# Kernel optimization log

Measured on AMD Instinct MI355X. Metric: run time of the kernel, lower is better.

The kernel has to match this reference:

```python
import jax, jax.numpy as jnp
import numpy as np

SIGMAS = (1.0, 10.0, 100.0, 1000.0)
EPS_RATIO = 1e-3  # lambda ridge term and ratio clip epsilon


def euclidsq(x, y):
    # squared pairwise Euclidean distances, [m, n]
    d = jnp.sum(x * x, axis=-1)[:, None] + jnp.sum(y * y, axis=-1)[None, :] - 2.0 * (x @ y.T)
    return jnp.maximum(d, 0.0)


def kmm_ratio(Kdede, Kdenu, lam):
    # original: inv(Kdede + lam*I) @ Kdenu @ ones == solve(A, Kdenu @ ones)
    n_de = Kdede.shape[0]
    A = Kdede + lam * jnp.eye(n_de, dtype=Kdede.dtype)
    B = jnp.sum(Kdenu, axis=1, keepdims=True)  # [n_de, 1]
    return jnp.linalg.solve(A, B)


def estimate_ratio(x_de, x_nu):
    # averaged KMM ratio over Gaussian kernels with fixed sigmas, then clip
    dsq_dede = euclidsq(x_de, x_de)
    dsq_denu = euclidsq(x_de, x_nu)
    ratio = 0.0
    for s in SIGMAS:
        inv2s2 = 1.0 / (2.0 * s * s)
        Kdede = jnp.exp(-dsq_dede * inv2s2)
        Kdenu = jnp.exp(-dsq_denu * inv2s2)
        ratio = ratio + kmm_ratio(Kdede, Kdenu, EPS_RATIO)
    ratio = ratio / len(SIGMAS)
    return jax.nn.relu(ratio) + EPS_RATIO  # clip_ratio=True


def reference(z1, z2, perm1, perm2):
    n, d = z1.shape
    z1s, z2s = z1[perm1], z2[perm2]
    # numerator ratio over full concatenated embeddings
    num_ratio = estimate_ratio(jnp.concatenate([z1, z2], axis=-1),
                               jnp.concatenate([z1s, z2s], axis=-1))
    num_ratio = 1.0 / num_ratio  # [n, 1]
    x_nu = jnp.concatenate([z2, z2], axis=-1)  # constant across samples

    def per_sample(z1_i):
        # x_de row j = concat(z1_i, z2_shuffled[j])
        x_de = jnp.concatenate([jnp.broadcast_to(z1_i, (n, d)), z2s], axis=-1)
        return jnp.sum(estimate_ratio(x_de, x_nu))

    denum_sums = jax.vmap(per_sample)(z1)  # [n]
    loss = jnp.sum(-jnp.log(num_ratio[:, 0] / denum_sums))
    return loss


def setup_inputs() -> dict:
    key = jax.random.key(0)
    k1, k2 = jax.random.split(key)
    n, d = 256, 128
    z1 = jax.random.normal(k1, (n, d), dtype=jnp.float32)
    z2 = jax.random.normal(k2, (n, d), dtype=jnp.float32)
    perm1 = jnp.arange(n, dtype=jnp.int32)
    perm2 = jnp.arange(n, dtype=jnp.int32)
    return {"z1": z1, "z2": z2, "perm1": perm1, "perm2": perm2}
```

## Files before the change

kernel.cpp:

```cpp
#include <hip/hip_runtime.h>
#include <math.h>

#define N 256
#define Dd 128

__device__ __forceinline__ double inv2s2_of(int s){
    return (s==0)?0.5:(s==1)?5.0e-3:(s==2)?5.0e-5:5.0e-7;
}

__device__ __forceinline__ void sweep32(double P[32][33], int tid){
    if (tid < 64){
        int r = tid & 31, cg = tid >> 5;
        for (int j = 0; j < 32; j++){
            double d    = P[j][j];
            double invd = 1.0 / d;
            double cr   = P[r][j];
            double s    = cr * invd;
            bool rj = (r == j);
            double nv[16];
            #pragma unroll
            for (int c = 0; c < 16; c++){
                int col = cg*16 + c;
                double pj = P[j][col];
                double v  = P[r][col];
                nv[c] = rj ? ((col == j) ? -invd : v * invd)
                           : ((col == j) ? s : v - s*pj);
            }
            #pragma unroll
            for (int c = 0; c < 16; c++) P[r][cg*16+c] = nv[c];
        }
        #pragma unroll
        for (int c = 0; c < 16; c++) P[r][cg*16+c] = -P[r][cg*16+c];
    }
}

__global__ void k_dist(const float* __restrict__ z1, const float* __restrict__ z2,
                       const int* __restrict__ p1, const int* __restrict__ p2,
                       double* __restrict__ Aden, double* __restrict__ Anum,
                       double* __restrict__ S0, float* __restrict__ M4,
                       float* __restrict__ U4, double* __restrict__ bnum){
    __shared__ float Xs[16][17], Ys[16][17];
    int w = blockIdx.z;
    int tx = threadIdx.x, ty = threadIdx.y;
    int row = blockIdx.y*16 + ty, col = blockIdx.x*16 + tx;
    const float *Xb[2], *Yb[2]; const int *Xp[2], *Yp[2]; int npair = 1;
    Xb[1]=0; Yb[1]=0; Xp[0]=0; Yp[0]=0; Xp[1]=0; Yp[1]=0;
    switch(w){
        case 0: Xb[0]=z1; Yb[0]=z1; Xb[1]=z2; Yb[1]=z2; npair=2; break;
        case 1: Xb[0]=z1; Yb[0]=z1; Yp[0]=p1; Xb[1]=z2; Yb[1]=z2; Yp[1]=p2; npair=2; break;
        case 2: Xb[0]=z2; Yb[0]=z2; Xp[0]=p2; Yp[0]=p2; break;
        case 3: Xb[0]=z2; Yb[0]=z2; Xp[0]=p2; break;
        default:Xb[0]=z1; Yb[0]=z2; break;
    }
    double acc = 0.0;
    for (int p = 0; p < npair; p++){
        const float* X = Xb[p]; const float* Y = Yb[p];
        int xr = blockIdx.y*16 + ty; if (Xp[p]) xr = Xp[p][xr];
        int yr = blockIdx.x*16 + ty; if (Yp[p]) yr = Yp[p][yr];
        for (int c = 0; c < Dd; c += 16){
            __syncthreads();
            Xs[ty][tx] = X[xr*Dd + c + tx];
            Ys[ty][tx] = Y[yr*Dd + c + tx];
            __syncthreads();
            #pragma unroll
            for (int t = 0; t < 16; t++){
                float d = Xs[ty][t] - Ys[tx][t];
                acc += (double)d * (double)d;
            }
        }
    }
    int o = row*N + col;
    if (w == 0){
        #pragma unroll
        for (int s = 0; s < 4; s++){
            double v = exp(-inv2s2_of(s)*acc);
            if (row == col) v += 1.0e-3;
            Anum[s*N*N + o] = v;
            S0[(4+s)*N*N + o] = v;
        }
    } else if (w == 1){
        #pragma unroll
        for (int s = 0; s < 4; s++){
            double v = exp(-inv2s2_of(s)*acc);
            v += __shfl_down(v, 8, 16);
            v += __shfl_down(v, 4, 16);
            v += __shfl_down(v, 2, 16);
            v += __shfl_down(v, 1, 16);
            if (tx == 0) atomicAdd(&bnum[s*N + row], v);
        }
    } else if (w == 2){
        #pragma unroll
        for (int s = 0; s < 4; s++){
            double v = exp(-inv2s2_of(s)*acc);
            if (row == col) v += 1.0e-3;
            Aden[s*N*N + o] = v;
            S0[s*N*N + o] = v;
        }
    } else if (w == 3){
        #pragma unroll
        for (int s = 0; s < 4; s++) M4[s*N*N + o] = (float)exp(-inv2s2_of(s)*acc);
    } else {
        #pragma unroll
        for (int s = 0; s < 4; s++) U4[s*N*N + o] = (float)exp(-inv2s2_of(s)*acc);
    }
}


__global__ void k_pivot0(const double* __restrict__ S0, double* __restrict__ Pg0){
    __shared__ double P[32][33];
    int mat = blockIdx.x;
    const double* S = S0 + (size_t)mat*65536;
    double* Pp = Pg0 + (size_t)mat*1024;
    int tid = threadIdx.x;
    #pragma unroll
    for (int l = 0; l < 4; l++){
        int e = tid + l*256; P[e>>5][e&31] = S[(size_t)(e>>5)*N + (e&31)];
    }
    __syncthreads();
    sweep32(P, tid);
    __syncthreads();
    #pragma unroll
    for (int l = 0; l < 4; l++){
        int e = tid + l*256; Pp[e] = P[e>>5][e&31];
    }
}

__global__ void k_step(const double* __restrict__ Ssrc, double* __restrict__ Sdst,
                       const double* __restrict__ PgS, double* __restrict__ PgD, int k){
    __shared__ double Pl[32][33], EJ[32][33], Cl[32][33], El[32][33];
    int bx = blockIdx.x, mat = blockIdx.y;
    const double* S = Ssrc + (size_t)mat*65536;
    double* D = Sdst + (size_t)mat*65536;
    const double* Pp = PgS + (size_t)mat*1024;
    int tid = threadIdx.x;
    int Kb = k*32;
    #pragma unroll
    for (int l = 0; l < 4; l++){
        int e = tid + l*256; Pl[e>>5][e&31] = Pp[e];
    }
    if (bx < 49){
        int I = bx / 7, J = bx % 7;
        int GI = ((I < k) ? I : I + 1) * 32;
        int GJ = ((J < k) ? J : J + 1) * 32;
        #pragma unroll
        for (int l = 0; l < 4; l++){
            int e = tid + l*256; int r = e >> 5, c = e & 31;
            El[r][c] = S[(size_t)(GI + r)*N + Kb + c];
            EJ[r][c] = S[(size_t)(GJ + r)*N + Kb + c];
        }
        __syncthreads();
        #pragma unroll
        for (int l = 0; l < 4; l++){
            int e = tid + l*256; int r = e >> 5, c = e & 31;
            double acc = 0.0;
            #pragma unroll
            for (int kk = 0; kk < 32; kk++) acc += EJ[r][kk] * Pl[kk][c];
            Cl[r][c] = acc;
        }
        __syncthreads();
        int pr = tid >> 4, pc = tid & 15;
        int r0 = 2*pr, c0 = 2*pc;
        double a00 = S[(size_t)(GI+r0)*N + GJ+c0];
        double a01 = S[(size_t)(GI+r0)*N + GJ+c0+1];
        double a10 = S[(size_t)(GI+r0+1)*N + GJ+c0];
        double a11 = S[(size_t)(GI+r0+1)*N + GJ+c0+1];
        #pragma unroll
        for (int kk = 0; kk < 32; kk++){
            double e0 = El[r0][kk],   e1 = El[r0+1][kk];
            double b0 = Cl[c0][kk],   b1 = Cl[c0+1][kk];
            a00 -= e0*b0; a01 -= e0*b1;
            a10 -= e1*b0; a11 -= e1*b1;
        }
        double* Dp = D + (size_t)(GI + r0)*N + GJ + c0;
        Dp[0]   = a00; Dp[1]   = a01;
        Dp[N]   = a10; Dp[N+1] = a11;
        if (I == k && J == k && k < 7){
            __syncthreads();
            El[r0][c0]   = a00; El[r0][c0+1]   = a01;
            El[r0+1][c0] = a10; El[r0+1][c0+1] = a11;
            __syncthreads();
            sweep32(El, tid);
            __syncthreads();
            double* Pd = PgD + (size_t)mat*1024;
            #pragma unroll
            for (int l = 0; l < 4; l++){
                int e = tid + l*256; Pd[e] = El[e>>5][e&31];
            }
        }
    } else {
        int T = bx - 49;
        int GT = ((T < k) ? T : T + 1) * 32;
        #pragma unroll
        for (int l = 0; l < 4; l++){
            int e = tid + l*256; int r = e >> 5, c = e & 31;
            El[r][c] = S[(size_t)(GT + r)*N + Kb + c];
        }
        __syncthreads();
        #pragma unroll
        for (int l = 0; l < 4; l++){
            int e = tid + l*256; int r = e >> 5, c = e & 31;
            double acc = 0.0;
            #pragma unroll
            for (int kk = 0; kk < 32; kk++) acc += El[r][kk] * Pl[kk][c];
            Cl[r][c] = acc;
        }
        __syncthreads();
        #pragma unroll
        for (int l = 0; l < 4; l++){
            int e = tid + l*256; int r = e >> 5, c = e & 31;
            D[(size_t)(GT + r)*N + Kb + c] = Cl[r][c];
        }
        #pragma unroll
        for (int l = 0; l < 4; l++){
            int e = tid + l*256; int cc = e >> 5, rr = e & 31;
            D[(size_t)(Kb + cc)*N + GT + rr] = Cl[rr][cc];
        }
        if (T == 0){
            #pragma unroll
            for (int l = 0; l < 4; l++){
                int e = tid + l*256; int i = e >> 5, j = e & 31;
                D[(size_t)(Kb + i)*N + Kb + j] = -Pl[i][j];
            }
        }
    }
}

__global__ void k_gemm_nt(const float* __restrict__ M4, const float* __restrict__ U4,
                          double* __restrict__ Bmat){
    int s = blockIdx.z;
    const float* Mp = M4 + s*N*N;
    const float* Up = U4 + s*N*N;
    double* Bp = Bmat + s*N*N;
    __shared__ float Ms[32][33], Us[32][33];
    int tx = threadIdx.x, ty = threadIdx.y;
    int tid = ty*16 + tx;
    int bj = blockIdx.y*32, bi = blockIdx.x*32;
    double a00=0, a01=0, a10=0, a11=0;
    for (int kc = 0; kc < N; kc += 32){
        __syncthreads();
        #pragma unroll
        for (int l = 0; l < 4; l++){
            int e = tid + l*256; int r = e >> 5, c = e & 31;
            Ms[r][c] = Mp[(bj+r)*N + kc + c];
            Us[r][c] = Up[(bi+r)*N + kc + c];
        }
        __syncthreads();
        #pragma unroll
        for (int k = 0; k < 32; k++){
            float x0 = Ms[2*ty][k], x1 = Ms[2*ty+1][k];
            float y0 = Us[2*tx][k], y1 = Us[2*tx+1][k];
            a00 += (double)x0*y0; a01 += (double)x0*y1;
            a10 += (double)x1*y0; a11 += (double)x1*y1;
        }
    }
    Bp[(bj+2*ty  )*N + bi+2*tx  ] = a00;
    Bp[(bj+2*ty  )*N + bi+2*tx+1] = a01;
    Bp[(bj+2*ty+1)*N + bi+2*tx  ] = a10;
    Bp[(bj+2*ty+1)*N + bi+2*tx+1] = a11;
}

__global__ void k_gemm_x0(const double* __restrict__ Sfin, const double* __restrict__ Bmat,
                          float* __restrict__ X0){
    int s = blockIdx.z;
    const double* Sp = Sfin + (size_t)s*N*N;
    const double* Bp = Bmat + s*N*N;
    float* Xp = X0 + s*N*N;
    __shared__ float Gs[32][33];
    __shared__ double Bs[32][33];
    int tx = threadIdx.x, ty = threadIdx.y;
    int tid = ty*16 + tx;
    int bj = blockIdx.y*32, bi = blockIdx.x*32;
    double a00=0, a01=0, a10=0, a11=0;
    for (int kc = 0; kc < N; kc += 32){
        __syncthreads();
        #pragma unroll
        for (int l = 0; l < 4; l++){
            int e = tid + l*256; int r = e >> 5, c = e & 31;
            Gs[r][c] = -(float)Sp[(size_t)(bj+r)*N + kc + c];
            Bs[r][c] = Bp[(kc+r)*N + bi + c];
        }
        __syncthreads();
        #pragma unroll
        for (int k = 0; k < 32; k++){
            float x0 = Gs[2*ty][k], x1 = Gs[2*ty+1][k];
            double y0 = Bs[k][2*tx], y1 = Bs[k][2*tx+1];
            a00 += (double)x0*y0; a01 += (double)x0*y1;
            a10 += (double)x1*y0; a11 += (double)x1*y1;
        }
    }
    Xp[(bj+2*ty  )*N + bi+2*tx  ] = (float)a00;
    Xp[(bj+2*ty  )*N + bi+2*tx+1] = (float)a01;
    Xp[(bj+2*ty+1)*N + bi+2*tx  ] = (float)a10;
    Xp[(bj+2*ty+1)*N + bi+2*tx+1] = (float)a11;
}

__global__ void k_gemm_r(const double* __restrict__ Aden, const float* __restrict__ X0,
                         const double* __restrict__ Bmat, float* __restrict__ Rm){
    int s = blockIdx.z;
    const double* Ap = Aden + s*N*N;
    const float* Xp = X0 + s*N*N;
    const double* Bp = Bmat + s*N*N;
    float* Rp = Rm + s*N*N;
    __shared__ double As[32][33];
    __shared__ float Xs[32][33];
    int tx = threadIdx.x, ty = threadIdx.y;
    int tid = ty*16 + tx;
    int bj = blockIdx.y*32, bi = blockIdx.x*32;
    double a00=0, a01=0, a10=0, a11=0;
    for (int kc = 0; kc < N; kc += 32){
        __syncthreads();
        #pragma unroll
        for (int l = 0; l < 4; l++){
            int e = tid + l*256; int r = e >> 5, c = e & 31;
            As[r][c] = Ap[(bj+r)*N + kc + c];
            Xs[r][c] = Xp[(kc+r)*N + bi + c];
        }
        __syncthreads();
        #pragma unroll
        for (int k = 0; k < 32; k++){
            double x0 = As[2*ty][k], x1 = As[2*ty+1][k];
            double y0 = (double)Xs[k][2*tx], y1 = (double)Xs[k][2*tx+1];
            a00 += x0*y0; a01 += x0*y1;
            a10 += x1*y0; a11 += x1*y1;
        }
    }
    int r0 = bj+2*ty, c0 = bi+2*tx;
    Rp[(r0  )*N + c0  ] = (float)(Bp[(r0  )*N + c0  ] - a00);
    Rp[(r0  )*N + c0+1] = (float)(Bp[(r0  )*N + c0+1] - a01);
    Rp[(r0+1)*N + c0  ] = (float)(Bp[(r0+1)*N + c0  ] - a10);
    Rp[(r0+1)*N + c0+1] = (float)(Bp[(r0+1)*N + c0+1] - a11);
}

__global__ void k_gemm_xl(const double* __restrict__ Sfin, const float* __restrict__ Rm,
                          const float* __restrict__ X0, double* __restrict__ dsum,
                          const double* __restrict__ Anum,
                          const double* __restrict__ bnum, float* __restrict__ rnum){
    __shared__ float Gs[32][33], Rs[32][33];
    __shared__ double cp[16][33];
    __shared__ double y0[256], rr2[256], bsh[256];
    int tx = threadIdx.x, ty = threadIdx.y;
    int tid = ty*16 + tx;
    if (blockIdx.y == 8){
        if (blockIdx.x >= 4) return;
        int s = blockIdx.x, j = tid;
        const double* Sn = Sfin + (size_t)(4+s)*N*N;
        const double* Ap = Anum + s*N*N;
        const double* bp = bnum + s*N;
        bsh[j] = bp[j];
        __syncthreads();
        double acc = 0;
        for (int k = 0; k < N; k++) acc -= Sn[(size_t)k*N+j] * bsh[k];
        y0[j] = acc;
        __syncthreads();
        acc = 0;
        for (int k = 0; k < N; k++) acc += Ap[(size_t)k*N+j] * y0[k];
        rr2[j] = bsh[j] - acc;
        __syncthreads();
        acc = 0;
        for (int k = 0; k < N; k++) acc -= Sn[(size_t)k*N+j] * rr2[k];
        rnum[s*N+j] = (float)(y0[j] + acc);
        return;
    }
    int bj = blockIdx.y*32, bi = blockIdx.x*32;
    int r0 = bj+2*ty, c0 = bi+2*tx;
    double s00=0, s01=0, s10=0, s11=0;
    for (int s = 0; s < 4; s++){
        const double* Sp = Sfin + (size_t)s*N*N;
        const float* Rp = Rm + s*N*N;
        const float* X0p = X0 + s*N*N;
        double a00=0, a01=0, a10=0, a11=0;
        for (int kc = 0; kc < N; kc += 32){
            __syncthreads();
            #pragma unroll
            for (int l = 0; l < 4; l++){
                int e = tid + l*256; int r = e >> 5, c = e & 31;
                Gs[r][c] = -(float)Sp[(size_t)(bj+r)*N + kc + c];
                Rs[r][c] = Rp[(kc+r)*N + bi + c];
            }
            __syncthreads();
            #pragma unroll
            for (int k = 0; k < 32; k++){
                float x0 = Gs[2*ty][k], x1 = Gs[2*ty+1][k];
                float y0v = Rs[k][2*tx], y1v = Rs[k][2*tx+1];
                a00 += (double)x0*y0v; a01 += (double)x0*y1v;
                a10 += (double)x1*y0v; a11 += (double)x1*y1v;
            }
        }
        s00 += (double)X0p[(r0  )*N + c0  ] + a00;
        s01 += (double)X0p[(r0  )*N + c0+1] + a01;
        s10 += (double)X0p[(r0+1)*N + c0  ] + a10;
        s11 += (double)X0p[(r0+1)*N + c0+1] + a11;
    }
    double v00 = (double)fmaxf((float)(0.25*s00), 0.f);
    double v01 = (double)fmaxf((float)(0.25*s01), 0.f);
    double v10 = (double)fmaxf((float)(0.25*s10), 0.f);
    double v11 = (double)fmaxf((float)(0.25*s11), 0.f);
    __syncthreads();
    cp[ty][2*tx]   = v00 + v10;
    cp[ty][2*tx+1] = v01 + v11;
    __syncthreads();
    if (tid < 32){
        double ssum = 0;
        #pragma unroll
        for (int t = 0; t < 16; t++) ssum += cp[t][tid];
        atomicAdd(&dsum[bi + tid], ssum);
    }
}

__global__ void k_loss2(const double* __restrict__ dsum, const float* __restrict__ rnum,
                        float* __restrict__ out){
    __shared__ double red[256];
    int i = threadIdx.x;
    double denum = dsum[i] + (double)N * 1.0e-3;
    float ravg = 0.25f*(rnum[0*N+i] + rnum[1*N+i] + rnum[2*N+i] + rnum[3*N+i]);
    double rn = (double)fmaxf(ravg, 0.f) + 1.0e-3;
    red[i] = log(rn) + log(denum);
    __syncthreads();
    for (int st = 128; st > 0; st >>= 1){
        if (i < st) red[i] += red[i + st];
        __syncthreads();
    }
    if (i == 0) out[0] = (float)red[0];
}

extern "C" void kernel_launch(void* const* d_in, const int* in_sizes, int n_in,
                              void* d_out, int out_size, void* d_ws, size_t ws_size,
                              hipStream_t stream) {
    (void)in_sizes; (void)n_in; (void)out_size; (void)ws_size;
    const float* z1 = (const float*)d_in[0];
    const float* z2 = (const float*)d_in[1];
    const int*   p1 = (const int*)d_in[2];
    const int*   p2 = (const int*)d_in[3];
    float* out = (float*)d_out;

    char* w = (char*)d_ws;
    size_t o = 0;
    auto carve = [&](size_t bytes) -> char* {
        char* p = w + o;
        o += (bytes + 255) & ~(size_t)255;
        return p;
    };
    double*   bnum = (double*) carve((size_t)4*N*sizeof(double));
    double*   dsum = (double*) carve((size_t)N*sizeof(double));
    size_t zbytes = o;
    double* Aden = (double*)carve((size_t)4*N*N*sizeof(double));
    double* Anum = (double*)carve((size_t)4*N*N*sizeof(double));
    float*  M4   = (float*) carve((size_t)4*N*N*sizeof(float));
    float*  U4   = (float*) carve((size_t)4*N*N*sizeof(float));
    double* Bmat = (double*)carve((size_t)4*N*N*sizeof(double));
    float*  X0   = (float*) carve((size_t)4*N*N*sizeof(float));
    float*  Rm   = (float*) carve((size_t)4*N*N*sizeof(float));
    float*  rnum = (float*) carve((size_t)4*N*sizeof(float));
    double* S0   = (double*)carve((size_t)8*N*N*sizeof(double));
    double* S1   = (double*)carve((size_t)8*N*N*sizeof(double));
    double* Pg0  = (double*)carve((size_t)8*32*32*sizeof(double));
    double* Pg1  = (double*)carve((size_t)8*32*32*sizeof(double));

    hipMemsetAsync(d_ws, 0, zbytes, stream);
    k_dist<<<dim3(16,16,5), dim3(16,16), 0, stream>>>(z1, z2, p1, p2,
                                                      Aden, Anum, S0, M4, U4, bnum);
    k_gemm_nt<<<dim3(8,8,4), dim3(16,16), 0, stream>>>(M4, U4, Bmat);
    k_pivot0<<<dim3(8), dim3(256), 0, stream>>>(S0, Pg0);
    for (int k = 0; k < 8; k++){
        double* src = (k & 1) ? S1 : S0;
        double* dst = (k & 1) ? S0 : S1;
        double* ps  = (k & 1) ? Pg1 : Pg0;
        double* pd  = (k & 1) ? Pg0 : Pg1;
        k_step<<<dim3(56,8), dim3(256), 0, stream>>>(src, dst, ps, pd, k);
    }
    k_gemm_x0<<<dim3(8,8,4), dim3(16,16), 0, stream>>>(S0, Bmat, X0);
    k_gemm_r<<<dim3(8,8,4), dim3(16,16), 0, stream>>>(Aden, X0, Bmat, Rm);
    k_gemm_xl<<<dim3(8,9), dim3(16,16), 0, stream>>>(S0, Rm, X0, dsum,
                                                     Anum, bnum, rnum);
    k_loss2<<<dim3(1), dim3(256), 0, stream>>>(dsum, rnum, out);
}
```

Baseline: 495.1 us.

## Drop iterative refinement pass, fuse pivot into gemm, and remove memset via partial sums

Removes the residual-refinement stage (the k_gemm_r and k_gemm_xl correction GEMMs and the Anum/Aden copies) and computes the solution with a single double-precision inverse-times-B GEMM followed by a reduction kernel. The first pivot sweep is folded into the k_gemm_nt launch as an extra z-slice, which also zeroes dsum. bnum atomics are replaced by per-block partial sums, so the memset goes away. Three launches and several large intermediate buffers are eliminated. The cost is dropping the refinement step, which may reduce solution accuracy for the ill-conditioned large-sigma kernels.

```diff
diff --git a/kernel.cpp b/kernel.cpp
--- a/kernel.cpp
+++ b/kernel.cpp
@@ -36,9 +36,8 @@
 
 __global__ void k_dist(const float* __restrict__ z1, const float* __restrict__ z2,
                        const int* __restrict__ p1, const int* __restrict__ p2,
-                       double* __restrict__ Aden, double* __restrict__ Anum,
                        double* __restrict__ S0, float* __restrict__ M4,
-                       float* __restrict__ U4, double* __restrict__ bnum){
+                       float* __restrict__ U4, double* __restrict__ bpart){
     __shared__ float Xs[16][17], Ys[16][17];
     int w = blockIdx.z;
     int tx = threadIdx.x, ty = threadIdx.y;
@@ -75,8 +74,7 @@
         for (int s = 0; s < 4; s++){
             double v = exp(-inv2s2_of(s)*acc);
             if (row == col) v += 1.0e-3;
-            Anum[s*N*N + o] = v;
-            S0[(4+s)*N*N + o] = v;
+            S0[(size_t)(4+s)*N*N + o] = v;
         }
     } else if (w == 1){
         #pragma unroll
@@ -86,15 +84,14 @@
             v += __shfl_down(v, 4, 16);
             v += __shfl_down(v, 2, 16);
             v += __shfl_down(v, 1, 16);
-            if (tx == 0) atomicAdd(&bnum[s*N + row], v);
+            if (tx == 0) bpart[((size_t)s*N + row)*16 + blockIdx.x] = v;
         }
     } else if (w == 2){
         #pragma unroll
         for (int s = 0; s < 4; s++){
             double v = exp(-inv2s2_of(s)*acc);
             if (row == col) v += 1.0e-3;
-            Aden[s*N*N + o] = v;
-            S0[s*N*N + o] = v;
+            S0[(size_t)s*N*N + o] = v;
         }
     } else if (w == 3){
         #pragma unroll
@@ -105,24 +102,59 @@
     }
 }
 
-
-__global__ void k_pivot0(const double* __restrict__ S0, double* __restrict__ Pg0){
+__global__ void k_gemm_nt(const float* __restrict__ M4, const float* __restrict__ U4,
+                          double* __restrict__ Bmat, const double* __restrict__ S0,
+                          double* __restrict__ Pg0, double* __restrict__ dsum){
+    __shared__ float Ms[32][33], Us[32][33];
     __shared__ double P[32][33];
-    int mat = blockIdx.x;
-    const double* S = S0 + (size_t)mat*65536;
-    double* Pp = Pg0 + (size_t)mat*1024;
-    int tid = threadIdx.x;
-    #pragma unroll
-    for (int l = 0; l < 4; l++){
-        int e = tid + l*256; P[e>>5][e&31] = S[(size_t)(e>>5)*N + (e&31)];
-    }
-    __syncthreads();
-    sweep32(P, tid);
-    __syncthreads();
-    #pragma unroll
-    for (int l = 0; l < 4; l++){
-        int e = tid + l*256; Pp[e] = P[e>>5][e&31];
-    }
+    int tx = threadIdx.x, ty = threadIdx.y;
+    int tid = ty*16 + tx;
+    if (blockIdx.z == 4){
+        if (blockIdx.y != 0) return;
+        int mat = blockIdx.x;
+        if (mat == 0) dsum[tid] = 0.0;
+        const double* S = S0 + (size_t)mat*65536;
+        #pragma unroll
+        for (int l = 0; l < 4; l++){
+            int e = tid + l*256; P[e>>5][e&31] = S[(size_t)(e>>5)*N + (e&31)];
+        }
+        __syncthreads();
+        sweep32(P, tid);
+        __syncthreads();
+        double* Pp = Pg0 + (size_t)mat*1024;
+        #pragma unroll
+        for (int l = 0; l < 4; l++){
+            int e = tid + l*256; Pp[e] = P[e>>5][e&31];
+        }
+        return;
+    }
+    int s = blockIdx.z;
+    const float* Mp = M4 + s*N*N;
+    const float* Up = U4 + s*N*N;
+    double* Bp = Bmat + s*N*N;
+    int bj = blockIdx.y*32, bi = blockIdx.x*32;
+    double a00=0, a01=0, a10=0, a11=0;
+    for (int kc = 0; kc < N; kc += 32){
+        __syncthreads();
+        #pragma unroll
+        for (int l = 0; l < 4; l++){
+            int e = tid + l*256; int r = e >> 5, c = e & 31;
+            Ms[r][c] = Mp[(bj+r)*N + kc + c];
+            Us[r][c] = Up[(bi+r)*N + kc + c];
+        }
+        __syncthreads();
+        #pragma unroll
+        for (int k = 0; k < 32; k++){
+            float x0 = Ms[2*ty][k], x1 = Ms[2*ty+1][k];
+            float y0 = Us[2*tx][k], y1 = Us[2*tx+1][k];
+            a00 += (double)x0*y0; a01 += (double)x0*y1;
+            a10 += (double)x1*y0; a11 += (double)x1*y1;
+        }
+    }
+    Bp[(bj+2*ty  )*N + bi+2*tx  ] = a00;
+    Bp[(bj+2*ty  )*N + bi+2*tx+1] = a01;
+    Bp[(bj+2*ty+1)*N + bi+2*tx  ] = a10;
+    Bp[(bj+2*ty+1)*N + bi+2*tx+1] = a11;
 }
 
 __global__ void k_step(const double* __restrict__ Ssrc, double* __restrict__ Sdst,
@@ -225,13 +257,13 @@
     }
 }
 
-__global__ void k_gemm_nt(const float* __restrict__ M4, const float* __restrict__ U4,
-                          double* __restrict__ Bmat){
+__global__ void k_x(const double* __restrict__ Sfin, const double* __restrict__ Bmat,
+                    float* __restrict__ Xm){
     int s = blockIdx.z;
-    const float* Mp = M4 + s*N*N;
-    const float* Up = U4 + s*N*N;
-    double* Bp = Bmat + s*N*N;
-    __shared__ float Ms[32][33], Us[32][33];
+    const double* Sp = Sfin + (size_t)s*N*N;
+    const double* Bp = Bmat + (size_t)s*N*N;
+    float* Xp = Xm + (size_t)s*N*N;
+    __shared__ double Gs[32][33], Bs[32][33];
     int tx = threadIdx.x, ty = threadIdx.y;
     int tid = ty*16 + tx;
     int bj = blockIdx.y*32, bi = blockIdx.x*32;
@@ -241,51 +273,16 @@
         #pragma unroll
         for (int l = 0; l < 4; l++){
             int e = tid + l*256; int r = e >> 5, c = e & 31;
-            Ms[r][c] = Mp[(bj+r)*N + kc + c];
-            Us[r][c] = Up[(bi+r)*N + kc + c];
+            Gs[r][c] = -Sp[(size_t)(bj+r)*N + kc + c];
+            Bs[r][c] = Bp[(size_t)(kc+r)*N + bi + c];
         }
         __syncthreads();
         #pragma unroll
         for (int k = 0; k < 32; k++){
-            float x0 = Ms[2*ty][k], x1 = Ms[2*ty+1][k];
-            float y0 = Us[2*tx][k], y1 = Us[2*tx+1][k];
-            a00 += (double)x0*y0; a01 += (double)x0*y1;
-            a10 += (double)x1*y0; a11 += (double)x1*y1;
-        }
-    }
-    Bp[(bj+2*ty  )*N + bi+2*tx  ] = a00;
-    Bp[(bj+2*ty  )*N + bi+2*tx+1] = a01;
-    Bp[(bj+2*ty+1)*N + bi+2*tx  ] = a10;
-    Bp[(bj+2*ty+1)*N + bi+2*tx+1] = a11;
-}
-
-__global__ void k_gemm_x0(const double* __restrict__ Sfin, const double* __restrict__ Bmat,
-                          float* __restrict__ X0){
-    int s = blockIdx.z;
-    const double* Sp = Sfin + (size_t)s*N*N;
-    const double* Bp = Bmat + s*N*N;
-    float* Xp = X0 + s*N*N;
-    __shared__ float Gs[32][33];
-    __shared__ double Bs[32][33];
-    int tx = threadIdx.x, ty = threadIdx.y;
-    int tid = ty*16 + tx;
-    int bj = blockIdx.y*32, bi = blockIdx.x*32;
-    double a00=0, a01=0, a10=0, a11=0;
-    for (int kc = 0; kc < N; kc += 32){
-        __syncthreads();
-        #pragma unroll
-        for (int l = 0; l < 4; l++){
-            int e = tid + l*256; int r = e >> 5, c = e & 31;
-            Gs[r][c] = -(float)Sp[(size_t)(bj+r)*N + kc + c];
-            Bs[r][c] = Bp[(kc+r)*N + bi + c];
-        }
-        __syncthreads();
-        #pragma unroll
-        for (int k = 0; k < 32; k++){
-            float x0 = Gs[2*ty][k], x1 = Gs[2*ty+1][k];
+            double x0 = Gs[2*ty][k], x1 = Gs[2*ty+1][k];
             double y0 = Bs[k][2*tx], y1 = Bs[k][2*tx+1];
-            a00 += (double)x0*y0; a01 += (double)x0*y1;
-            a10 += (double)x1*y0; a11 += (double)x1*y1;
+            a00 += x0*y0; a01 += x0*y1;
+            a10 += x1*y0; a11 += x1*y1;
         }
     }
     Xp[(bj+2*ty  )*N + bi+2*tx  ] = (float)a00;
@@ -294,116 +291,40 @@
     Xp[(bj+2*ty+1)*N + bi+2*tx+1] = (float)a11;
 }
 
-__global__ void k_gemm_r(const double* __restrict__ Aden, const float* __restrict__ X0,
-                         const double* __restrict__ Bmat, float* __restrict__ Rm){
-    int s = blockIdx.z;
-    const double* Ap = Aden + s*N*N;
-    const float* Xp = X0 + s*N*N;
-    const double* Bp = Bmat + s*N*N;
-    float* Rp = Rm + s*N*N;
-    __shared__ double As[32][33];
-    __shared__ float Xs[32][33];
-    int tx = threadIdx.x, ty = threadIdx.y;
-    int tid = ty*16 + tx;
-    int bj = blockIdx.y*32, bi = blockIdx.x*32;
-    double a00=0, a01=0, a10=0, a11=0;
-    for (int kc = 0; kc < N; kc += 32){
-        __syncthreads();
-        #pragma unroll
-        for (int l = 0; l < 4; l++){
-            int e = tid + l*256; int r = e >> 5, c = e & 31;
-            As[r][c] = Ap[(bj+r)*N + kc + c];
-            Xs[r][c] = Xp[(kc+r)*N + bi + c];
-        }
-        __syncthreads();
-        #pragma unroll
-        for (int k = 0; k < 32; k++){
-            double x0 = As[2*ty][k], x1 = As[2*ty+1][k];
-            double y0 = (double)Xs[k][2*tx], y1 = (double)Xs[k][2*tx+1];
-            a00 += x0*y0; a01 += x0*y1;
-            a10 += x1*y0; a11 += x1*y1;
-        }
-    }
-    int r0 = bj+2*ty, c0 = bi+2*tx;
-    Rp[(r0  )*N + c0  ] = (float)(Bp[(r0  )*N + c0  ] - a00);
-    Rp[(r0  )*N + c0+1] = (float)(Bp[(r0  )*N + c0+1] - a01);
-    Rp[(r0+1)*N + c0  ] = (float)(Bp[(r0+1)*N + c0  ] - a10);
-    Rp[(r0+1)*N + c0+1] = (float)(Bp[(r0+1)*N + c0+1] - a11);
-}
-
-__global__ void k_gemm_xl(const double* __restrict__ Sfin, const float* __restrict__ Rm,
-                          const float* __restrict__ X0, double* __restrict__ dsum,
-                          const double* __restrict__ Anum,
-                          const double* __restrict__ bnum, float* __restrict__ rnum){
-    __shared__ float Gs[32][33], Rs[32][33];
-    __shared__ double cp[16][33];
-    __shared__ double y0[256], rr2[256], bsh[256];
-    int tx = threadIdx.x, ty = threadIdx.y;
-    int tid = ty*16 + tx;
-    if (blockIdx.y == 8){
-        if (blockIdx.x >= 4) return;
-        int s = blockIdx.x, j = tid;
+__global__ void k_red(const float* __restrict__ Xm, const double* __restrict__ Sfin,
+                      const double* __restrict__ bpart, double* __restrict__ dsum,
+                      float* __restrict__ rnum){
+    __shared__ double cp[32][33];
+    __shared__ double bsh[256];
+    int b = blockIdx.x, tid = threadIdx.x;
+    if (b < 64){
+        int bj = (b >> 3)*32, bi = (b & 7)*32;
+        #pragma unroll
+        for (int l = 0; l < 4; l++){
+            int e = tid + l*256; int r = e >> 5, c = e & 31;
+            int o = (bj + r)*N + bi + c;
+            float x = Xm[0*N*N + o] + Xm[1*N*N + o] + Xm[2*N*N + o] + Xm[3*N*N + o];
+            cp[r][c] = (double)fmaxf(0.25f*x, 0.f);
+        }
+        __syncthreads();
+        if (tid < 32){
+            double ssum = 0;
+            #pragma unroll
+            for (int r = 0; r < 32; r++) ssum += cp[r][tid];
+            atomicAdd(&dsum[bi + tid], ssum);
+        }
+    } else {
+        int s = b - 64, j = tid;
         const double* Sn = Sfin + (size_t)(4+s)*N*N;
-        const double* Ap = Anum + s*N*N;
-        const double* bp = bnum + s*N;
-        bsh[j] = bp[j];
-        __syncthreads();
+        const double* bp = bpart + (size_t)s*N*16;
         double acc = 0;
-        for (int k = 0; k < N; k++) acc -= Sn[(size_t)k*N+j] * bsh[k];
-        y0[j] = acc;
-        __syncthreads();
-        acc = 0;
-        for (int k = 0; k < N; k++) acc += Ap[(size_t)k*N+j] * y0[k];
-        rr2[j] = bsh[j] - acc;
-        __syncthreads();
-        acc = 0;
-        for (int k = 0; k < N; k++) acc -= Sn[(size_t)k*N+j] * rr2[k];
-        rnum[s*N+j] = (float)(y0[j] + acc);
-        return;
-    }
-    int bj = blockIdx.y*32, bi = blockIdx.x*32;
-    int r0 = bj+2*ty, c0 = bi+2*tx;
-    double s00=0, s01=0, s10=0, s11=0;
-    for (int s = 0; s < 4; s++){
-        const double* Sp = Sfin + (size_t)s*N*N;
-        const float* Rp = Rm + s*N*N;
-        const float* X0p = X0 + s*N*N;
-        double a00=0, a01=0, a10=0, a11=0;
-        for (int kc = 0; kc < N; kc += 32){
-            __syncthreads();
-            #pragma unroll
-            for (int l = 0; l < 4; l++){
-                int e = tid + l*256; int r = e >> 5, c = e & 31;
-                Gs[r][c] = -(float)Sp[(size_t)(bj+r)*N + kc + c];
-                Rs[r][c] = Rp[(kc+r)*N + bi + c];
-            }
-            __syncthreads();
-            #pragma unroll
-            for (int k = 0; k < 32; k++){
-                float x0 = Gs[2*ty][k], x1 = Gs[2*ty+1][k];
-                float y0v = Rs[k][2*tx], y1v = Rs[k][2*tx+1];
-                a00 += (double)x0*y0v; a01 += (double)x0*y1v;
-                a10 += (double)x1*y0v; a11 += (double)x1*y1v;
-            }
-        }
-        s00 += (double)X0p[(r0  )*N + c0  ] + a00;
-        s01 += (double)X0p[(r0  )*N + c0+1] + a01;
-        s10 += (double)X0p[(r0+1)*N + c0  ] + a10;
-        s11 += (double)X0p[(r0+1)*N + c0+1] + a11;
-    }
-    double v00 = (double)fmaxf((float)(0.25*s00), 0.f);
-    double v01 = (double)fmaxf((float)(0.25*s01), 0.f);
-    double v10 = (double)fmaxf((float)(0.25*s10), 0.f);
-    double v11 = (double)fmaxf((float)(0.25*s11), 0.f);
-    __syncthreads();
-    cp[ty][2*tx]   = v00 + v10;
-    cp[ty][2*tx+1] = v01 + v11;
-    __syncthreads();
-    if (tid < 32){
-        double ssum = 0;
-        #pragma unroll
-        for (int t = 0; t < 16; t++) ssum += cp[t][tid];
-        atomicAdd(&dsum[bi + tid], ssum);
+        #pragma unroll
+        for (int t = 0; t < 16; t++) acc += bp[j*16 + t];
+        bsh[j] = acc;
+        __syncthreads();
+        double y = 0;
+        for (int k = 0; k < N; k++) y -= Sn[(size_t)k*N + j] * bsh[k];
+        rnum[s*N + j] = (float)y;
     }
 }
 
@@ -440,27 +361,21 @@
         o += (bytes + 255) & ~(size_t)255;
         return p;
     };
-    double*   bnum = (double*) carve((size_t)4*N*sizeof(double));
-    double*   dsum = (double*) carve((size_t)N*sizeof(double));
-    size_t zbytes = o;
-    double* Aden = (double*)carve((size_t)4*N*N*sizeof(double));
-    double* Anum = (double*)carve((size_t)4*N*N*sizeof(double));
-    float*  M4   = (float*) carve((size_t)4*N*N*sizeof(float));
-    float*  U4   = (float*) carve((size_t)4*N*N*sizeof(float));
-    double* Bmat = (double*)carve((size_t)4*N*N*sizeof(double));
-    float*  X0   = (float*) carve((size_t)4*N*N*sizeof(float));
-    float*  Rm   = (float*) carve((size_t)4*N*N*sizeof(float));
-    float*  rnum = (float*) carve((size_t)4*N*sizeof(float));
-    double* S0   = (double*)carve((size_t)8*N*N*sizeof(double));
-    double* S1   = (double*)carve((size_t)8*N*N*sizeof(double));
-    double* Pg0  = (double*)carve((size_t)8*32*32*sizeof(double));
-    double* Pg1  = (double*)carve((size_t)8*32*32*sizeof(double));
-
-    hipMemsetAsync(d_ws, 0, zbytes, stream);
+    double* bpart = (double*)carve((size_t)4*N*16*sizeof(double));
+    double* dsum  = (double*)carve((size_t)N*sizeof(double));
+    float*  M4    = (float*) carve((size_t)4*N*N*sizeof(float));
+    float*  U4    = (float*) carve((size_t)4*N*N*sizeof(float));
+    double* Bmat  = (double*)carve((size_t)4*N*N*sizeof(double));
+    float*  Xm    = (float*) carve((size_t)4*N*N*sizeof(float));
+    float*  rnum  = (float*) carve((size_t)4*N*sizeof(float));
+    double* S0    = (double*)carve((size_t)8*N*N*sizeof(double));
+    double* S1    = (double*)carve((size_t)8*N*N*sizeof(double));
+    double* Pg0   = (double*)carve((size_t)8*32*32*sizeof(double));
+    double* Pg1   = (double*)carve((size_t)8*32*32*sizeof(double));
+
     k_dist<<<dim3(16,16,5), dim3(16,16), 0, stream>>>(z1, z2, p1, p2,
-                                                      Aden, Anum, S0, M4, U4, bnum);
-    k_gemm_nt<<<dim3(8,8,4), dim3(16,16), 0, stream>>>(M4, U4, Bmat);
-    k_pivot0<<<dim3(8), dim3(256), 0, stream>>>(S0, Pg0);
+                                                      S0, M4, U4, bpart);
+    k_gemm_nt<<<dim3(8,8,5), dim3(16,16), 0, stream>>>(M4, U4, Bmat, S0, Pg0, dsum);
     for (int k = 0; k < 8; k++){
         double* src = (k & 1) ? S1 : S0;
         double* dst = (k & 1) ? S0 : S1;
@@ -468,9 +383,7 @@
         double* pd  = (k & 1) ? Pg0 : Pg1;
         k_step<<<dim3(56,8), dim3(256), 0, stream>>>(src, dst, ps, pd, k);
     }
-    k_gemm_x0<<<dim3(8,8,4), dim3(16,16), 0, stream>>>(S0, Bmat, X0);
-    k_gemm_r<<<dim3(8,8,4), dim3(16,16), 0, stream>>>(Aden, X0, Bmat, Rm);
-    k_gemm_xl<<<dim3(8,9), dim3(16,16), 0, stream>>>(S0, Rm, X0, dsum,
-                                                     Anum, bnum, rnum);
+    k_x<<<dim3(8,8,4), dim3(16,16), 0, stream>>>(S0, Bmat, Xm);
+    k_red<<<dim3(68), dim3(256), 0, stream>>>(Xm, S0, bpart, dsum, rnum);
     k_loss2<<<dim3(1), dim3(256), 0, stream>>>(dsum, rnum, out);
 }
```

Result: faster. 439.3 us (-11.3%).
